# Kernel optimization log

Hardware: AMD Instinct MI355X
Metric: run time of the kernel (lower is better)

Reference implementation:

```python
import jax, jax.numpy as jnp
import numpy as np

N = 50000
E = 800000
HEADS = 4
C = 64  # per-head channels
IN = 256
NEG_SLOPE = 0.2


def setup_inputs() -> dict:
    key = jax.random.key(0)
    k = jax.random.split(key, 6)
    x = jax.random.normal(k[0], (N, IN), dtype=jnp.float32)
    edge_index = jax.random.randint(k[1], (2, E), 0, N, dtype=jnp.int64)
    # Glorot-ish scale for weights
    W = jax.random.normal(k[2], (IN, HEADS * C), dtype=jnp.float32) * (1.0 / np.sqrt(IN))
    att_src = jax.random.normal(k[3], (HEADS, C), dtype=jnp.float32) * (1.0 / np.sqrt(C))
    att_dst = jax.random.normal(k[4], (HEADS, C), dtype=jnp.float32) * (1.0 / np.sqrt(C))
    bias = jax.random.normal(k[5], (HEADS * C,), dtype=jnp.float32) * 0.02
    return {"x": x, "edge_index": edge_index, "W": W, "att_src": att_src,
            "att_dst": att_dst, "bias": bias}


def _gat_forward(x, edge_index, W, att_src, att_dst, bias):
    n = x.shape[0]
    h = (x @ W).reshape(n, HEADS, C)  # [N, H, C]

    # add self loops (PyG default add_self_loops=True)
    loop = jnp.arange(n, dtype=edge_index.dtype)
    src = jnp.concatenate([edge_index[0], loop])  # [E+N]
    dst = jnp.concatenate([edge_index[1], loop])

    # per-node attention contributions  [N, H]
    a_src = jnp.einsum('nhc,hc->nh', h, att_src)
    a_dst = jnp.einsum('nhc,hc->nh', h, att_dst)

    # edge logits with leaky relu  [E+N, H]
    logits = a_src[src] + a_dst[dst]
    logits = jnp.where(logits >= 0, logits, NEG_SLOPE * logits)

    # segment softmax over destination neighborhoods
    seg_max = jax.ops.segment_max(logits, dst, num_segments=n)  # [N, H]
    seg_max = jnp.where(jnp.isfinite(seg_max), seg_max, 0.0)
    ex = jnp.exp(logits - seg_max[dst])
    denom = jax.ops.segment_sum(ex, dst, num_segments=n)  # [N, H]
    alpha = ex / (denom[dst] + 1e-16)  # [E+N, H]

    # weighted scatter-add of source messages
    msgs = alpha[:, :, None] * h[src]  # [E+N, H, C]
    out = jax.ops.segment_sum(msgs, dst, num_segments=n)  # [N, H, C]
    out = out.reshape(n, HEADS * C) + bias
    return jax.nn.relu(out)


def reference(x, edge_index, W, att_src, att_dst, bias):
    return _gat_forward(x, edge_index, W, att_src, att_dst, bias)
```

## Files before the change

### kernel.cpp

```cpp
#include <hip/hip_runtime.h>
#include <hip/hip_bf16.h>
#include <math.h>

#define NEG 0.2f
#define BSH 6
#define EPB 2048

typedef __attribute__((ext_vector_type(4))) float f4;
typedef __attribute__((ext_vector_type(8))) short s8;

__device__ __forceinline__ short f2bf(float f) {
    unsigned u = __float_as_uint(f);
    u += 0x7fff + ((u >> 16) & 1);
    return (short)(u >> 16);
}
__device__ __forceinline__ unsigned pk2(float a, float b) {
    union { __hip_bfloat162 h; unsigned u; } c;
    c.h = __float22bfloat162_rn(make_float2(a, b));
    return c.u;
}
__device__ __forceinline__ float bf2f(unsigned short s) {
    return __uint_as_float(((unsigned)s) << 16);
}

__global__ __launch_bounds__(256) void prep_count(
    const float* __restrict__ W, short* __restrict__ Wt, int* __restrict__ off,
    const int* __restrict__ ei, int* __restrict__ hist2d,
    int E, int N, int NBUCK, int NB, int Etot)
{
    const int blk = blockIdx.x, t = threadIdx.x;
    if (blk < 256) {
        int id = blk * 256 + t;
        int n = id >> 8, k = id & 255;
        Wt[id] = f2bf(W[k * 256 + n]);
        if (id == 0) off[N] = Etot;
        return;
    }
    extern __shared__ int lh[];
    const int cblk = blk - 256;
    for (int b = t; b < NBUCK; b += 256) lh[b] = 0;
    __syncthreads();
    const int e0 = cblk * EPB;
    if (e0 + EPB <= E) {
#pragma unroll
        for (int i = 0; i < EPB / 1024; ++i) {
            int e = e0 + i * 1024 + t * 4;
            int4 d = *(const int4*)(ei + E + e);
            atomicAdd(&lh[d.x >> BSH], 1);
            atomicAdd(&lh[d.y >> BSH], 1);
            atomicAdd(&lh[d.z >> BSH], 1);
            atomicAdd(&lh[d.w >> BSH], 1);
        }
    } else {
        for (int i = 0; i < EPB / 256; ++i) {
            int e = e0 + i * 256 + t;
            if (e < Etot) {
                int dte = (e < E) ? ei[E + e] : (e - E);
                atomicAdd(&lh[dte >> BSH], 1);
            }
        }
    }
    __syncthreads();
    for (int b = t; b < NBUCK; b += 256) hist2d[b * NB + cblk] = lh[b];
}

__global__ __launch_bounds__(1024) void scan1(const int* __restrict__ src,
                                              int* __restrict__ dstT,
                                              int* __restrict__ bsum,
                                              int Ntot, int NB, int NBUCK)
{
    __shared__ int wsum[16], wexc[16];
    const int t = threadIdx.x, lane = t & 63, w = t >> 6;
    const int idx = blockIdx.x * 1024 + t;
    int v = (idx < Ntot) ? src[idx] : 0;
    int val = v;
#pragma unroll
    for (int o = 1; o < 64; o <<= 1) {
        int u = __shfl_up(val, o);
        if (lane >= o) val += u;
    }
    if (lane == 63) wsum[w] = val;
    __syncthreads();
    if (t < 16) {
        int s = wsum[t];
#pragma unroll
        for (int o = 1; o < 16; o <<= 1) {
            int u = __shfl_up(s, o, 16);
            if (t >= o) s += u;
        }
        wexc[t] = s - wsum[t];
        if (t == 15) bsum[blockIdx.x] = s;
    }
    __syncthreads();
    if (idx < Ntot) {
        int b = idx / NB, cblk = idx - b * NB;
        dstT[(size_t)cblk * NBUCK + b] = wexc[w] + val - v;
    }
}

__device__ __forceinline__ void bexc_scan_wave(const int* __restrict__ bsum,
                                               int* bexc_l, int NCH, int t)
{
    if (t < 64) {
        int carry = 0;
        for (int base = 0; base < NCH; base += 64) {
            int i = base + t;
            int v = (i < NCH) ? bsum[i] : 0;
            int val = v;
#pragma unroll
            for (int o = 1; o < 64; o <<= 1) {
                int u = __shfl_up(val, o);
                if (t >= o) val += u;
            }
            if (i < NCH) bexc_l[i] = carry + val - v;
            carry += __shfl(val, 63);
        }
    }
}

__global__ __launch_bounds__(512) void gemm_scatter(
    const float* __restrict__ x, const short* __restrict__ Wt,
    const float* __restrict__ att_src, const float* __restrict__ att_dst,
    short* __restrict__ hb, float* __restrict__ a_src_n,
    float* __restrict__ a_dst_n, int M, int GB,
    const int* __restrict__ ei, const int* __restrict__ scannedT,
    const int* __restrict__ bsum, unsigned* __restrict__ bucketed,
    int E, int N, int NBUCK, int NB, int NCH)
{
    extern __shared__ __align__(16) char smem[];
    const int t = threadIdx.x;

    if (blockIdx.x >= GB) {
        int* bexc_l = (int*)smem;
        int* lcur   = (int*)smem + 384;
        const int cblk = blockIdx.x - GB;
        bexc_scan_wave(bsum, bexc_l, NCH, t);
        __syncthreads();
        const int* srow = scannedT + (size_t)cblk * NBUCK;
        for (int b = t; b < NBUCK; b += 512)
            lcur[b] = srow[b] + bexc_l[(b * NB + cblk) >> 10];
        __syncthreads();
        const int e0 = cblk * EPB, Etot = E + N;
        if (e0 + EPB <= E) {
            int e = e0 + t * 4;
            int4 s4 = *(const int4*)(ei + e);
            int4 d4 = *(const int4*)(ei + E + e);
            int p0 = atomicAdd(&lcur[d4.x >> BSH], 1);
            bucketed[p0] = (unsigned)s4.x | ((unsigned)(d4.x & 63) << 20);
            int p1 = atomicAdd(&lcur[d4.y >> BSH], 1);
            bucketed[p1] = (unsigned)s4.y | ((unsigned)(d4.y & 63) << 20);
            int p2 = atomicAdd(&lcur[d4.z >> BSH], 1);
            bucketed[p2] = (unsigned)s4.z | ((unsigned)(d4.z & 63) << 20);
            int p3 = atomicAdd(&lcur[d4.w >> BSH], 1);
            bucketed[p3] = (unsigned)s4.w | ((unsigned)(d4.w & 63) << 20);
        } else {
            for (int i = 0; i < EPB / 512; ++i) {
                int e = e0 + i * 512 + t;
                if (e < Etot) {
                    int src, dte;
                    if (e < E) { src = ei[e]; dte = ei[E + e]; }
                    else       { src = e - E; dte = src; }
                    int pos = atomicAdd(&lcur[dte >> BSH], 1);
                    bucketed[pos] = (unsigned)src | ((unsigned)(dte & 63) << 20);
                }
            }
        }
        return;
    }

    short (*xs)[128][32] = (short (*)[128][32])smem;
    const int lane = t & 63, wv = t >> 6;
    const int wr = wv >> 2;
    const int hd = wv & 3;
    const int quad = lane >> 4, l15 = lane & 15;
    const int n0 = blockIdx.x * 128;

    const int row = t >> 2, kq = t & 3;
    const bool okr = (n0 + row) < M;
    const float* xp = x + (size_t)(n0 + row) * 256 + kq * 8;

    const short* wbase = Wt + (size_t)(hd * 64 + l15) * 256 + quad * 8;

    f4 acc[4][4];
#pragma unroll
    for (int i = 0; i < 4; ++i)
#pragma unroll
        for (int j = 0; j < 4; ++j) acc[i][j] = (f4)(0.f);

    float4 v0 = {}, v1 = {};
    if (okr) { const float4* p = (const float4*)xp; v0 = p[0]; v1 = p[1]; }

    s8 af[4];
#pragma unroll
    for (int i = 0; i < 4; ++i)
        af[i] = *(const s8*)(wbase + (size_t)(i * 16) * 256);

    int buf = 0;
#pragma unroll
    for (int ks = 0; ks < 8; ++ks) {
        uint4 u = { pk2(v0.x, v0.y), pk2(v0.z, v0.w), pk2(v1.x, v1.y), pk2(v1.z, v1.w) };
        *(uint4*)&xs[buf][row][kq * 8] = u;
        __syncthreads();

        if (ks < 7 && okr) {
            const float4* p = (const float4*)(xp + (ks + 1) * 32);
            v0 = p[0]; v1 = p[1];
        }

        s8 afn[4];
        if (ks < 7) {
#pragma unroll
            for (int i = 0; i < 4; ++i)
                afn[i] = *(const s8*)(wbase + (size_t)(i * 16) * 256 + (ks + 1) * 32);
        }

        s8 bf[4];
#pragma unroll
        for (int j = 0; j < 4; ++j)
            bf[j] = *(const s8*)&xs[buf][wr * 64 + j * 16 + l15][quad * 8];
#pragma unroll
        for (int i = 0; i < 4; ++i)
#pragma unroll
            for (int j = 0; j < 4; ++j)
                acc[i][j] = __builtin_amdgcn_mfma_f32_16x16x32_bf16(af[i], bf[j], acc[i][j], 0, 0, 0);

        if (ks < 7) {
#pragma unroll
            for (int i = 0; i < 4; ++i) af[i] = afn[i];
        }
        buf ^= 1;
    }

    float asv[4][4], adv[4][4];
#pragma unroll
    for (int i = 0; i < 4; ++i)
#pragma unroll
        for (int rr = 0; rr < 4; ++rr) {
            asv[i][rr] = att_src[hd * 64 + i * 16 + quad * 4 + rr];
            adv[i][rr] = att_dst[hd * 64 + i * 16 + quad * 4 + rr];
        }

#pragma unroll
    for (int j = 0; j < 4; ++j) {
        const int node = n0 + wr * 64 + j * 16 + l15;
        const bool ok = node < M;
        float ps = 0.f, pd = 0.f;
#pragma unroll
        for (int i = 0; i < 4; ++i)
#pragma unroll
            for (int rr = 0; rr < 4; ++rr) {
                float v = acc[i][j][rr];
                ps = fmaf(v, asv[i][rr], ps);
                pd = fmaf(v, adv[i][rr], pd);
            }
        ps += __shfl_xor(ps, 16); ps += __shfl_xor(ps, 32);
        pd += __shfl_xor(pd, 16); pd += __shfl_xor(pd, 32);
        if (ok && quad == 0) {
            a_src_n[node * 4 + hd] = ps;
            a_dst_n[node * 4 + hd] = pd;
        }
        if (ok) {
#pragma unroll
            for (int i = 0; i < 4; ++i) {
                uint2 pk = make_uint2(pk2(acc[i][j][0], acc[i][j][1]),
                                      pk2(acc[i][j][2], acc[i][j][3]));
                *(uint2*)&hb[(size_t)node * 256 + hd * 64 + i * 16 + quad * 4] = pk;
            }
        }
    }
}

__global__ __launch_bounds__(512) void csr_build(
    const unsigned* __restrict__ bucketed, const int* __restrict__ scannedT,
    const int* __restrict__ bsum, int* __restrict__ off, int* __restrict__ csr,
    int N, int NB, int NBUCK, int Etot, int NCH)
{
    __shared__ unsigned est[2048];
    __shared__ int ldeg8[8][64], lcur8[8][64], loff[64], bexc_l[384];
    const int t = threadIdx.x, wv = t >> 6, b = blockIdx.x;

    bexc_scan_wave(bsum, bexc_l, NCH, t);
    ldeg8[t >> 6][t & 63] = 0;
    __syncthreads();

    const int gbase = scannedT[b] + bexc_l[(b * NB) >> 10];
    int gend;
    if (b + 1 == NBUCK) gend = Etot;
    else gend = scannedT[b + 1] + bexc_l[((b + 1) * NB) >> 10];
    int cnt = gend - gbase;
    if (cnt > 2048) cnt = 2048;

    for (int i = t; i < cnt; i += 512) {
        unsigned en = bucketed[gbase + i];
        est[i] = en;
        atomicAdd(&ldeg8[wv][en >> 20], 1);
    }
    __syncthreads();
    if (t < 64) {
        int d0 = ldeg8[0][t], d1 = ldeg8[1][t], d2 = ldeg8[2][t], d3 = ldeg8[3][t];
        int d4 = ldeg8[4][t], d5 = ldeg8[5][t], d6 = ldeg8[6][t], d7 = ldeg8[7][t];
        int tot = d0 + d1 + d2 + d3 + d4 + d5 + d6 + d7;
        int val = tot;
#pragma unroll
        for (int o = 1; o < 64; o <<= 1) {
            int u = __shfl_up(val, o);
            if (t >= o) val += u;
        }
        int excl = val - tot;
        loff[t] = excl;
        int c = excl;
        lcur8[0][t] = c; c += d0;
        lcur8[1][t] = c; c += d1;
        lcur8[2][t] = c; c += d2;
        lcur8[3][t] = c; c += d3;
        lcur8[4][t] = c; c += d4;
        lcur8[5][t] = c; c += d5;
        lcur8[6][t] = c; c += d6;
        lcur8[7][t] = c;
    }
    __syncthreads();
    for (int i = t; i < cnt; i += 512) {
        unsigned en = est[i];
        int pos = atomicAdd(&lcur8[wv][en >> 20], 1);
        csr[gbase + pos] = (int)(en & 0xFFFFF);
    }
    if (t < 64) {
        int n = (b << BSH) + t;
        if (n < N) off[n] = gbase + loff[t];
    }
}

__global__ __launch_bounds__(256) void aggregate(const short* __restrict__ hb,
                                                 const float* __restrict__ a_src_n,
                                                 const float* __restrict__ a_dst_n,
                                                 const int* __restrict__ off,
                                                 const int* __restrict__ csr,
                                                 const float* __restrict__ bias,
                                                 float* __restrict__ out, int N)
{
    __shared__ float lds_w[4][64][4];
    __shared__ int   lds_s[4][64];
    const int wv = threadIdx.x >> 6;
    const int lane = threadIdx.x & 63;
    const int half = lane >> 5, l31 = lane & 31;
    const int n = blockIdx.x * 4 + wv;
    if (n >= N) return;

    const int base = off[n];
    const int d = off[n + 1] - base;
    const float4 ad = *(const float4*)(a_dst_n + 4 * n);
    const int hl = l31 >> 3;

    float acc[8] = {0.f, 0.f, 0.f, 0.f, 0.f, 0.f, 0.f, 0.f};
    float4 sum = make_float4(0.f, 0.f, 0.f, 0.f);
    const uint4* hp = (const uint4*)hb;

    for (int c0 = 0; c0 < d; c0 += 64) {
        int j = c0 + lane;
        int s = 0;
        float4 w4 = make_float4(0.f, 0.f, 0.f, 0.f);
        if (j < d) {
            s = csr[base + j];
            float4 as = *(const float4*)(a_src_n + 4 * s);
            float lx = as.x + ad.x; lx = lx >= 0.f ? lx : NEG * lx;
            float ly = as.y + ad.y; ly = ly >= 0.f ? ly : NEG * ly;
            float lz = as.z + ad.z; lz = lz >= 0.f ? lz : NEG * lz;
            float lw = as.w + ad.w; lw = lw >= 0.f ? lw : NEG * lw;
            w4 = make_float4(__expf(lx), __expf(ly), __expf(lz), __expf(lw));
        }
        sum.x += w4.x; sum.y += w4.y; sum.z += w4.z; sum.w += w4.w;
        *(float4*)&lds_w[wv][lane][0] = w4;
        lds_s[wv][lane] = s;
        __builtin_amdgcn_wave_barrier();

        const int cl = (d - c0) < 64 ? (d - c0) : 64;
        int jj = 0;
        for (; jj + 4 <= cl; jj += 4) {
            int   s0 = lds_s[wv][jj + half];
            int   s1 = lds_s[wv][jj + 2 + half];
            float w0 = lds_w[wv][jj + half][hl];
            float w1 = lds_w[wv][jj + 2 + half][hl];
            uint4 v0 = hp[(size_t)s0 * 32 + l31];
            uint4 v1 = hp[(size_t)s1 * 32 + l31];
            acc[0] = fmaf(w0, bf2f((unsigned short)(v0.x & 0xffff)), acc[0]);
            acc[1] = fmaf(w0, bf2f((unsigned short)(v0.x >> 16)),    acc[1]);
            acc[2] = fmaf(w0, bf2f((unsigned short)(v0.y & 0xffff)), acc[2]);
            acc[3] = fmaf(w0, bf2f((unsigned short)(v0.y >> 16)),    acc[3]);
            acc[4] = fmaf(w0, bf2f((unsigned short)(v0.z & 0xffff)), acc[4]);
            acc[5] = fmaf(w0, bf2f((unsigned short)(v0.z >> 16)),    acc[5]);
            acc[6] = fmaf(w0, bf2f((unsigned short)(v0.w & 0xffff)), acc[6]);
            acc[7] = fmaf(w0, bf2f((unsigned short)(v0.w >> 16)),    acc[7]);
            acc[0] = fmaf(w1, bf2f((unsigned short)(v1.x & 0xffff)), acc[0]);
            acc[1] = fmaf(w1, bf2f((unsigned short)(v1.x >> 16)),    acc[1]);
            acc[2] = fmaf(w1, bf2f((unsigned short)(v1.y & 0xffff)), acc[2]);
            acc[3] = fmaf(w1, bf2f((unsigned short)(v1.y >> 16)),    acc[3]);
            acc[4] = fmaf(w1, bf2f((unsigned short)(v1.z & 0xffff)), acc[4]);
            acc[5] = fmaf(w1, bf2f((unsigned short)(v1.z >> 16)),    acc[5]);
            acc[6] = fmaf(w1, bf2f((unsigned short)(v1.w & 0xffff)), acc[6]);
            acc[7] = fmaf(w1, bf2f((unsigned short)(v1.w >> 16)),    acc[7]);
        }
        for (; jj < cl; jj += 2) {
            int   s0 = lds_s[wv][jj + half];
            float w0 = lds_w[wv][jj + half][hl];
            uint4 v0 = hp[(size_t)s0 * 32 + l31];
            acc[0] = fmaf(w0, bf2f((unsigned short)(v0.x & 0xffff)), acc[0]);
            acc[1] = fmaf(w0, bf2f((unsigned short)(v0.x >> 16)),    acc[1]);
            acc[2] = fmaf(w0, bf2f((unsigned short)(v0.y & 0xffff)), acc[2]);
            acc[3] = fmaf(w0, bf2f((unsigned short)(v0.y >> 16)),    acc[3]);
            acc[4] = fmaf(w0, bf2f((unsigned short)(v0.z & 0xffff)), acc[4]);
            acc[5] = fmaf(w0, bf2f((unsigned short)(v0.z >> 16)),    acc[5]);
            acc[6] = fmaf(w0, bf2f((unsigned short)(v0.w & 0xffff)), acc[6]);
            acc[7] = fmaf(w0, bf2f((unsigned short)(v0.w >> 16)),    acc[7]);
        }
        __builtin_amdgcn_wave_barrier();
    }

#pragma unroll
    for (int k = 0; k < 8; ++k) acc[k] += __shfl_xor(acc[k], 32);

#pragma unroll
    for (int o = 32; o > 0; o >>= 1) {
        sum.x += __shfl_xor(sum.x, o);
        sum.y += __shfl_xor(sum.y, o);
        sum.z += __shfl_xor(sum.z, o);
        sum.w += __shfl_xor(sum.w, o);
    }
    float sh = (hl & 2) ? ((hl & 1) ? sum.w : sum.z) : ((hl & 1) ? sum.y : sum.x);
    float ih = 1.f / (sh + 1e-16f);

    if (half == 0) {
        const float4* bp = (const float4*)bias + l31 * 2;
        float4 b0 = bp[0], b1 = bp[1];
        float4 o0, o1;
        o0.x = fmaxf(fmaf(acc[0], ih, b0.x), 0.f);
        o0.y = fmaxf(fmaf(acc[1], ih, b0.y), 0.f);
        o0.z = fmaxf(fmaf(acc[2], ih, b0.z), 0.f);
        o0.w = fmaxf(fmaf(acc[3], ih, b0.w), 0.f);
        o1.x = fmaxf(fmaf(acc[4], ih, b1.x), 0.f);
        o1.y = fmaxf(fmaf(acc[5], ih, b1.y), 0.f);
        o1.z = fmaxf(fmaf(acc[6], ih, b1.z), 0.f);
        o1.w = fmaxf(fmaf(acc[7], ih, b1.w), 0.f);
        float4* op = (float4*)(out + (size_t)n * 256) + l31 * 2;
        op[0] = o0;
        op[1] = o1;
    }
}

extern "C" void kernel_launch(void* const* d_in, const int* in_sizes, int n_in,
                              void* d_out, int out_size, void* d_ws, size_t ws_size,
                              hipStream_t stream)
{
    const float* x       = (const float*)d_in[0];
    const int*   ei      = (const int*)d_in[1];
    const float* W       = (const float*)d_in[2];
    const float* att_src = (const float*)d_in[3];
    const float* att_dst = (const float*)d_in[4];
    const float* bias    = (const float*)d_in[5];
    float* out = (float*)d_out;

    const int N = in_sizes[0] / 256;
    const int E = in_sizes[1] / 2;
    const int Etot = E + N;
    const int NBUCK = (N + 63) >> BSH;
    const int NB = (Etot + EPB - 1) / EPB;
    const int Ntot = NBUCK * NB;
    const int NCH = (Ntot + 1023) / 1024;
    const int GB = (N + 127) / 128;

    char* p = (char*)d_ws;
    short*    hb      = (short*)p;    p += (size_t)N * 256 * sizeof(short);
    short*    Wt      = (short*)p;    p += 256 * 256 * sizeof(short);
    float*    a_src_n = (float*)p;    p += (size_t)N * 4 * sizeof(float);
    float*    a_dst_n = (float*)p;    p += (size_t)N * 4 * sizeof(float);
    int*      hist2d  = (int*)p;      p += (size_t)Ntot * sizeof(int);
    int*      scannedT= (int*)p;      p += (size_t)Ntot * sizeof(int);
    int*      bsum    = (int*)p;      p += 1024 * sizeof(int);
    int*      off     = (int*)p;      p += (size_t)(N + 1) * sizeof(int);
    unsigned* bucketed= (unsigned*)p; p += (size_t)Etot * sizeof(unsigned);
    int*      csr     = (int*)p;      p += (size_t)Etot * sizeof(int);

    prep_count<<<256 + NB, 256, NBUCK * sizeof(int), stream>>>(
        W, Wt, off, ei, hist2d, E, N, NBUCK, NB, Etot);
    scan1<<<NCH, 1024, 0, stream>>>(hist2d, scannedT, bsum, Ntot, NB, NBUCK);
    gemm_scatter<<<GB + NB, 512, 16384, stream>>>(
        x, Wt, att_src, att_dst, hb, a_src_n, a_dst_n, N, GB,
        ei, scannedT, bsum, bucketed, E, N, NBUCK, NB, NCH);
    csr_build<<<NBUCK, 512, 0, stream>>>(bucketed, scannedT, bsum, off, csr,
                                         N, NB, NBUCK, Etot, NCH);
    aggregate<<<(N + 3) / 4, 256, 0, stream>>>(hb, a_src_n, a_dst_n, off, csr,
                                               bias, out, N);
}
```

Baseline: 217.4 us.

## Fuse preprocessing and GEMM kernels into one cooperative persistent kernel

Replaces the four launches before aggregation (weight transpose and histogram, scan, GEMM plus scatter, CSR build) with a single cooperative kernel. The phases are separated by grid-wide syncs, and each phase's work units are distributed over a persistent grid sized from occupancy, capped at NBUCK. The scan now handles two elements per thread with 512 threads. The goal is to remove kernel launch gaps and tail effects between the small phases. The cost is grid-sync overhead, and the GEMM now runs in a persistent loop over a grid capped at NBUCK blocks rather than its own full-size launch, which may reduce parallelism. The old multi-kernel path is kept as a fallback if the cooperative launch fails.

```diff
diff --git a/kernel.cpp b/kernel.cpp
--- a/kernel.cpp
+++ b/kernel.cpp
@@ -1,6 +1,9 @@
 #include <hip/hip_runtime.h>
 #include <hip/hip_bf16.h>
+#include <hip/hip_cooperative_groups.h>
 #include <math.h>
+
+namespace cg = cooperative_groups;
 
 #define NEG 0.2f
 #define BSH 6
@@ -21,81 +24,6 @@
 }
 __device__ __forceinline__ float bf2f(unsigned short s) {
     return __uint_as_float(((unsigned)s) << 16);
-}
-
-__global__ __launch_bounds__(256) void prep_count(
-    const float* __restrict__ W, short* __restrict__ Wt, int* __restrict__ off,
-    const int* __restrict__ ei, int* __restrict__ hist2d,
-    int E, int N, int NBUCK, int NB, int Etot)
-{
-    const int blk = blockIdx.x, t = threadIdx.x;
-    if (blk < 256) {
-        int id = blk * 256 + t;
-        int n = id >> 8, k = id & 255;
-        Wt[id] = f2bf(W[k * 256 + n]);
-        if (id == 0) off[N] = Etot;
-        return;
-    }
-    extern __shared__ int lh[];
-    const int cblk = blk - 256;
-    for (int b = t; b < NBUCK; b += 256) lh[b] = 0;
-    __syncthreads();
-    const int e0 = cblk * EPB;
-    if (e0 + EPB <= E) {
-#pragma unroll
-        for (int i = 0; i < EPB / 1024; ++i) {
-            int e = e0 + i * 1024 + t * 4;
-            int4 d = *(const int4*)(ei + E + e);
-            atomicAdd(&lh[d.x >> BSH], 1);
-            atomicAdd(&lh[d.y >> BSH], 1);
-            atomicAdd(&lh[d.z >> BSH], 1);
-            atomicAdd(&lh[d.w >> BSH], 1);
-        }
-    } else {
-        for (int i = 0; i < EPB / 256; ++i) {
-            int e = e0 + i * 256 + t;
-            if (e < Etot) {
-                int dte = (e < E) ? ei[E + e] : (e - E);
-                atomicAdd(&lh[dte >> BSH], 1);
-            }
-        }
-    }
-    __syncthreads();
-    for (int b = t; b < NBUCK; b += 256) hist2d[b * NB + cblk] = lh[b];
-}
-
-__global__ __launch_bounds__(1024) void scan1(const int* __restrict__ src,
-                                              int* __restrict__ dstT,
-                                              int* __restrict__ bsum,
-                                              int Ntot, int NB, int NBUCK)
-{
-    __shared__ int wsum[16], wexc[16];
-    const int t = threadIdx.x, lane = t & 63, w = t >> 6;
-    const int idx = blockIdx.x * 1024 + t;
-    int v = (idx < Ntot) ? src[idx] : 0;
-    int val = v;
-#pragma unroll
-    for (int o = 1; o < 64; o <<= 1) {
-        int u = __shfl_up(val, o);
-        if (lane >= o) val += u;
-    }
-    if (lane == 63) wsum[w] = val;
-    __syncthreads();
-    if (t < 16) {
-        int s = wsum[t];
-#pragma unroll
-        for (int o = 1; o < 16; o <<= 1) {
-            int u = __shfl_up(s, o, 16);
-            if (t >= o) s += u;
-        }
-        wexc[t] = s - wsum[t];
-        if (t == 15) bsum[blockIdx.x] = s;
-    }
-    __syncthreads();
-    if (idx < Ntot) {
-        int b = idx / NB, cblk = idx - b * NB;
-        dstT[(size_t)cblk * NBUCK + b] = wexc[w] + val - v;
-    }
 }
 
 __device__ __forceinline__ void bexc_scan_wave(const int* __restrict__ bsum,
@@ -118,67 +46,22 @@
     }
 }
 
-__global__ __launch_bounds__(512) void gemm_scatter(
+__device__ __forceinline__ void gemm_body(
+    char* smem, int t, int n0,
     const float* __restrict__ x, const short* __restrict__ Wt,
     const float* __restrict__ att_src, const float* __restrict__ att_dst,
     short* __restrict__ hb, float* __restrict__ a_src_n,
-    float* __restrict__ a_dst_n, int M, int GB,
-    const int* __restrict__ ei, const int* __restrict__ scannedT,
-    const int* __restrict__ bsum, unsigned* __restrict__ bucketed,
-    int E, int N, int NBUCK, int NB, int NCH)
-{
-    extern __shared__ __align__(16) char smem[];
-    const int t = threadIdx.x;
-
-    if (blockIdx.x >= GB) {
-        int* bexc_l = (int*)smem;
-        int* lcur   = (int*)smem + 384;
-        const int cblk = blockIdx.x - GB;
-        bexc_scan_wave(bsum, bexc_l, NCH, t);
-        __syncthreads();
-        const int* srow = scannedT + (size_t)cblk * NBUCK;
-        for (int b = t; b < NBUCK; b += 512)
-            lcur[b] = srow[b] + bexc_l[(b * NB + cblk) >> 10];
-        __syncthreads();
-        const int e0 = cblk * EPB, Etot = E + N;
-        if (e0 + EPB <= E) {
-            int e = e0 + t * 4;
-            int4 s4 = *(const int4*)(ei + e);
-            int4 d4 = *(const int4*)(ei + E + e);
-            int p0 = atomicAdd(&lcur[d4.x >> BSH], 1);
-            bucketed[p0] = (unsigned)s4.x | ((unsigned)(d4.x & 63) << 20);
-            int p1 = atomicAdd(&lcur[d4.y >> BSH], 1);
-            bucketed[p1] = (unsigned)s4.y | ((unsigned)(d4.y & 63) << 20);
-            int p2 = atomicAdd(&lcur[d4.z >> BSH], 1);
-            bucketed[p2] = (unsigned)s4.z | ((unsigned)(d4.z & 63) << 20);
-            int p3 = atomicAdd(&lcur[d4.w >> BSH], 1);
-            bucketed[p3] = (unsigned)s4.w | ((unsigned)(d4.w & 63) << 20);
-        } else {
-            for (int i = 0; i < EPB / 512; ++i) {
-                int e = e0 + i * 512 + t;
-                if (e < Etot) {
-                    int src, dte;
-                    if (e < E) { src = ei[e]; dte = ei[E + e]; }
-                    else       { src = e - E; dte = src; }
-                    int pos = atomicAdd(&lcur[dte >> BSH], 1);
-                    bucketed[pos] = (unsigned)src | ((unsigned)(dte & 63) << 20);
-                }
-            }
-        }
-        return;
-    }
-
+    float* __restrict__ a_dst_n, int M)
+{
     short (*xs)[128][32] = (short (*)[128][32])smem;
     const int lane = t & 63, wv = t >> 6;
     const int wr = wv >> 2;
     const int hd = wv & 3;
     const int quad = lane >> 4, l15 = lane & 15;
-    const int n0 = blockIdx.x * 128;
 
     const int row = t >> 2, kq = t & 3;
     const bool okr = (n0 + row) < M;
     const float* xp = x + (size_t)(n0 + row) * 256 + kq * 8;
-
     const short* wbase = Wt + (size_t)(hd * 64 + l15) * 256 + quad * 8;
 
     f4 acc[4][4];
@@ -206,14 +89,12 @@
             const float4* p = (const float4*)(xp + (ks + 1) * 32);
             v0 = p[0]; v1 = p[1];
         }
-
         s8 afn[4];
         if (ks < 7) {
 #pragma unroll
             for (int i = 0; i < 4; ++i)
                 afn[i] = *(const s8*)(wbase + (size_t)(i * 16) * 256 + (ks + 1) * 32);
         }
-
         s8 bf[4];
 #pragma unroll
         for (int j = 0; j < 4; ++j)
@@ -223,7 +104,6 @@
 #pragma unroll
             for (int j = 0; j < 4; ++j)
                 acc[i][j] = __builtin_amdgcn_mfma_f32_16x16x32_bf16(af[i], bf[j], acc[i][j], 0, 0, 0);
-
         if (ks < 7) {
 #pragma unroll
             for (int i = 0; i < 4; ++i) af[i] = afn[i];
@@ -239,7 +119,6 @@
             asv[i][rr] = att_src[hd * 64 + i * 16 + quad * 4 + rr];
             adv[i][rr] = att_dst[hd * 64 + i * 16 + quad * 4 + rr];
         }
-
 #pragma unroll
     for (int j = 0; j < 4; ++j) {
         const int node = n0 + wr * 64 + j * 16 + l15;
@@ -270,17 +149,62 @@
     }
 }
 
-__global__ __launch_bounds__(512) void csr_build(
+__device__ __forceinline__ void scatter_body(
+    char* smem, int t, int cblk,
+    const int* __restrict__ ei, const int* __restrict__ scannedT,
+    const int* __restrict__ bsum, unsigned* __restrict__ bucketed,
+    int E, int N, int NBUCK, int NB, int NCH)
+{
+    int* bexc_l = (int*)smem;
+    int* lcur   = (int*)smem + 384;
+    bexc_scan_wave(bsum, bexc_l, NCH, t);
+    __syncthreads();
+    const int* srow = scannedT + (size_t)cblk * NBUCK;
+    for (int b = t; b < NBUCK; b += 512)
+        lcur[b] = srow[b] + bexc_l[(b * NB + cblk) >> 10];
+    __syncthreads();
+    const int e0 = cblk * EPB, Etot = E + N;
+    if (e0 + EPB <= E) {
+        int e = e0 + t * 4;
+        int4 s4 = *(const int4*)(ei + e);
+        int4 d4 = *(const int4*)(ei + E + e);
+        int p0 = atomicAdd(&lcur[d4.x >> BSH], 1);
+        bucketed[p0] = (unsigned)s4.x | ((unsigned)(d4.x & 63) << 20);
+        int p1 = atomicAdd(&lcur[d4.y >> BSH], 1);
+        bucketed[p1] = (unsigned)s4.y | ((unsigned)(d4.y & 63) << 20);
+        int p2 = atomicAdd(&lcur[d4.z >> BSH], 1);
+        bucketed[p2] = (unsigned)s4.z | ((unsigned)(d4.z & 63) << 20);
+        int p3 = atomicAdd(&lcur[d4.w >> BSH], 1);
+        bucketed[p3] = (unsigned)s4.w | ((unsigned)(d4.w & 63) << 20);
+    } else {
+        for (int i = 0; i < EPB / 512; ++i) {
+            int e = e0 + i * 512 + t;
+            if (e < Etot) {
+                int src, dte;
+                if (e < E) { src = ei[e]; dte = ei[E + e]; }
+                else       { src = e - E; dte = src; }
+                int pos = atomicAdd(&lcur[dte >> BSH], 1);
+                bucketed[pos] = (unsigned)src | ((unsigned)(dte & 63) << 20);
+            }
+        }
+    }
+}
+
+__device__ __forceinline__ void csr_body(
+    char* smem, int t, int b,
     const unsigned* __restrict__ bucketed, const int* __restrict__ scannedT,
     const int* __restrict__ bsum, int* __restrict__ off, int* __restrict__ csr,
     int N, int NB, int NBUCK, int Etot, int NCH)
 {
-    __shared__ unsigned est[2048];
-    __shared__ int ldeg8[8][64], lcur8[8][64], loff[64], bexc_l[384];
-    const int t = threadIdx.x, wv = t >> 6, b = blockIdx.x;
+    unsigned* est = (unsigned*)smem;
+    int* ldeg8  = (int*)(smem + 8192);
+    int* lcur8  = (int*)(smem + 10240);
+    int* loff   = (int*)(smem + 12288);
+    int* bexc_l = (int*)(smem + 12544);
+    const int wv = t >> 6;
 
     bexc_scan_wave(bsum, bexc_l, NCH, t);
-    ldeg8[t >> 6][t & 63] = 0;
+    ldeg8[(t >> 6) * 64 + (t & 63)] = 0;
     __syncthreads();
 
     const int gbase = scannedT[b] + bexc_l[(b * NB) >> 10];
@@ -293,12 +217,12 @@
     for (int i = t; i < cnt; i += 512) {
         unsigned en = bucketed[gbase + i];
         est[i] = en;
-        atomicAdd(&ldeg8[wv][en >> 20], 1);
+        atomicAdd(&ldeg8[wv * 64 + (en >> 20)], 1);
     }
     __syncthreads();
     if (t < 64) {
-        int d0 = ldeg8[0][t], d1 = ldeg8[1][t], d2 = ldeg8[2][t], d3 = ldeg8[3][t];
-        int d4 = ldeg8[4][t], d5 = ldeg8[5][t], d6 = ldeg8[6][t], d7 = ldeg8[7][t];
+        int d0 = ldeg8[0 * 64 + t], d1 = ldeg8[1 * 64 + t], d2 = ldeg8[2 * 64 + t], d3 = ldeg8[3 * 64 + t];
+        int d4 = ldeg8[4 * 64 + t], d5 = ldeg8[5 * 64 + t], d6 = ldeg8[6 * 64 + t], d7 = ldeg8[7 * 64 + t];
         int tot = d0 + d1 + d2 + d3 + d4 + d5 + d6 + d7;
         int val = tot;
 #pragma unroll
@@ -309,25 +233,229 @@
         int excl = val - tot;
         loff[t] = excl;
         int c = excl;
-        lcur8[0][t] = c; c += d0;
-        lcur8[1][t] = c; c += d1;
-        lcur8[2][t] = c; c += d2;
-        lcur8[3][t] = c; c += d3;
-        lcur8[4][t] = c; c += d4;
-        lcur8[5][t] = c; c += d5;
-        lcur8[6][t] = c; c += d6;
-        lcur8[7][t] = c;
+        lcur8[0 * 64 + t] = c; c += d0;
+        lcur8[1 * 64 + t] = c; c += d1;
+        lcur8[2 * 64 + t] = c; c += d2;
+        lcur8[3 * 64 + t] = c; c += d3;
+        lcur8[4 * 64 + t] = c; c += d4;
+        lcur8[5 * 64 + t] = c; c += d5;
+        lcur8[6 * 64 + t] = c; c += d6;
+        lcur8[7 * 64 + t] = c;
     }
     __syncthreads();
     for (int i = t; i < cnt; i += 512) {
         unsigned en = est[i];
-        int pos = atomicAdd(&lcur8[wv][en >> 20], 1);
+        int pos = atomicAdd(&lcur8[wv * 64 + (en >> 20)], 1);
         csr[gbase + pos] = (int)(en & 0xFFFFF);
     }
     if (t < 64) {
         int n = (b << BSH) + t;
         if (n < N) off[n] = gbase + loff[t];
     }
+}
+
+__global__ __launch_bounds__(512) void mega(
+    const float* __restrict__ x, const float* __restrict__ W,
+    short* __restrict__ Wt,
+    const float* __restrict__ att_src, const float* __restrict__ att_dst,
+    short* __restrict__ hb, float* __restrict__ a_src_n, float* __restrict__ a_dst_n,
+    const int* __restrict__ ei, int* __restrict__ hist2d, int* __restrict__ scannedT,
+    int* __restrict__ bsum, int* __restrict__ off, unsigned* __restrict__ bucketed,
+    int* __restrict__ csr,
+    int N, int E, int Etot, int NBUCK, int NB, int Ntot, int NCH, int GB)
+{
+    extern __shared__ __align__(16) char smem[];
+    cg::grid_group gg = cg::this_grid();
+    const int t = threadIdx.x;
+    const int NBLK = gridDim.x;
+
+    for (int u = blockIdx.x; u < 128 + NB; u += NBLK) {
+        __syncthreads();
+        if (u < 128) {
+            int id = u * 512 + t;
+            int n = id >> 8, k = id & 255;
+            Wt[id] = f2bf(W[k * 256 + n]);
+            if (id == 0) off[N] = Etot;
+        } else {
+            int* lh = (int*)smem;
+            const int cblk = u - 128;
+            for (int b = t; b < NBUCK; b += 512) lh[b] = 0;
+            __syncthreads();
+            const int e0 = cblk * EPB;
+            if (e0 + EPB <= E) {
+                int e = e0 + t * 4;
+                int4 d = *(const int4*)(ei + E + e);
+                atomicAdd(&lh[d.x >> BSH], 1);
+                atomicAdd(&lh[d.y >> BSH], 1);
+                atomicAdd(&lh[d.z >> BSH], 1);
+                atomicAdd(&lh[d.w >> BSH], 1);
+            } else {
+                for (int i = 0; i < EPB / 512; ++i) {
+                    int e = e0 + i * 512 + t;
+                    if (e < Etot) {
+                        int dte = (e < E) ? ei[E + e] : (e - E);
+                        atomicAdd(&lh[dte >> BSH], 1);
+                    }
+                }
+            }
+            __syncthreads();
+            for (int b = t; b < NBUCK; b += 512) hist2d[b * NB + cblk] = lh[b];
+        }
+    }
+    __threadfence();
+    gg.sync();
+
+    for (int u = blockIdx.x; u < NCH + GB; u += NBLK) {
+        __syncthreads();
+        if (u < NCH) {
+            int* wsum = (int*)smem;
+            int* wexc = (int*)smem + 8;
+            const int lane = t & 63, w = t >> 6;
+            int base = u << 10;
+            int i0 = base + 2 * t;
+            int v0 = (i0 < Ntot) ? hist2d[i0] : 0;
+            int v1 = (i0 + 1 < Ntot) ? hist2d[i0 + 1] : 0;
+            int pv = v0 + v1;
+            int val = pv;
+#pragma unroll
+            for (int o = 1; o < 64; o <<= 1) { int s2 = __shfl_up(val, o); if (lane >= o) val += s2; }
+            if (lane == 63) wsum[w] = val;
+            __syncthreads();
+            if (t < 8) {
+                int s = wsum[t];
+#pragma unroll
+                for (int o = 1; o < 8; o <<= 1) { int s2 = __shfl_up(s, o, 8); if (t >= o) s += s2; }
+                wexc[t] = s - wsum[t];
+                if (t == 7) bsum[u] = s;
+            }
+            __syncthreads();
+            int excl = wexc[w] + val - pv;
+            if (i0 < Ntot) { int b = i0 / NB, cb = i0 - b * NB; scannedT[(size_t)cb * NBUCK + b] = excl; }
+            if (i0 + 1 < Ntot) { int idx = i0 + 1; int b = idx / NB, cb = idx - b * NB; scannedT[(size_t)cb * NBUCK + b] = excl + v0; }
+        } else {
+            gemm_body(smem, t, (u - NCH) * 128, x, Wt, att_src, att_dst,
+                      hb, a_src_n, a_dst_n, N);
+        }
+    }
+    __threadfence();
+    gg.sync();
+
+    for (int u = blockIdx.x; u < NB; u += NBLK) {
+        __syncthreads();
+        scatter_body(smem, t, u, ei, scannedT, bsum, bucketed, E, N, NBUCK, NB, NCH);
+    }
+    __threadfence();
+    gg.sync();
+
+    for (int u = blockIdx.x; u < NBUCK; u += NBLK) {
+        __syncthreads();
+        csr_body(smem, t, u, bucketed, scannedT, bsum, off, csr, N, NB, NBUCK, Etot, NCH);
+    }
+}
+
+__global__ __launch_bounds__(256) void prep_count(
+    const float* __restrict__ W, short* __restrict__ Wt, int* __restrict__ off,
+    const int* __restrict__ ei, int* __restrict__ hist2d,
+    int E, int N, int NBUCK, int NB, int Etot)
+{
+    const int blk = blockIdx.x, t = threadIdx.x;
+    if (blk < 256) {
+        int id = blk * 256 + t;
+        int n = id >> 8, k = id & 255;
+        Wt[id] = f2bf(W[k * 256 + n]);
+        if (id == 0) off[N] = Etot;
+        return;
+    }
+    extern __shared__ int lh[];
+    const int cblk = blk - 256;
+    for (int b = t; b < NBUCK; b += 256) lh[b] = 0;
+    __syncthreads();
+    const int e0 = cblk * EPB;
+    if (e0 + EPB <= E) {
+#pragma unroll
+        for (int i = 0; i < EPB / 1024; ++i) {
+            int e = e0 + i * 1024 + t * 4;
+            int4 d = *(const int4*)(ei + E + e);
+            atomicAdd(&lh[d.x >> BSH], 1);
+            atomicAdd(&lh[d.y >> BSH], 1);
+            atomicAdd(&lh[d.z >> BSH], 1);
+            atomicAdd(&lh[d.w >> BSH], 1);
+        }
+    } else {
+        for (int i = 0; i < EPB / 256; ++i) {
+            int e = e0 + i * 256 + t;
+            if (e < Etot) {
+                int dte = (e < E) ? ei[E + e] : (e - E);
+                atomicAdd(&lh[dte >> BSH], 1);
+            }
+        }
+    }
+    __syncthreads();
+    for (int b = t; b < NBUCK; b += 256) hist2d[b * NB + cblk] = lh[b];
+}
+
+__global__ __launch_bounds__(1024) void scan1(const int* __restrict__ src,
+                                              int* __restrict__ dstT,
+                                              int* __restrict__ bsum,
+                                              int Ntot, int NB, int NBUCK)
+{
+    __shared__ int wsum[16], wexc[16];
+    const int t = threadIdx.x, lane = t & 63, w = t >> 6;
+    const int idx = blockIdx.x * 1024 + t;
+    int v = (idx < Ntot) ? src[idx] : 0;
+    int val = v;
+#pragma unroll
+    for (int o = 1; o < 64; o <<= 1) {
+        int u = __shfl_up(val, o);
+        if (lane >= o) val += u;
+    }
+    if (lane == 63) wsum[w] = val;
+    __syncthreads();
+    if (t < 16) {
+        int s = wsum[t];
+#pragma unroll
+        for (int o = 1; o < 16; o <<= 1) {
+            int u = __shfl_up(s, o, 16);
+            if (t >= o) s += u;
+        }
+        wexc[t] = s - wsum[t];
+        if (t == 15) bsum[blockIdx.x] = s;
+    }
+    __syncthreads();
+    if (idx < Ntot) {
+        int b = idx / NB, cblk = idx - b * NB;
+        dstT[(size_t)cblk * NBUCK + b] = wexc[w] + val - v;
+    }
+}
+
+__global__ __launch_bounds__(512) void gemm_scatter(
+    const float* __restrict__ x, const short* __restrict__ Wt,
+    const float* __restrict__ att_src, const float* __restrict__ att_dst,
+    short* __restrict__ hb, float* __restrict__ a_src_n,
+    float* __restrict__ a_dst_n, int M, int GB,
+    const int* __restrict__ ei, const int* __restrict__ scannedT,
+    const int* __restrict__ bsum, unsigned* __restrict__ bucketed,
+    int E, int N, int NBUCK, int NB, int NCH)
+{
+    extern __shared__ __align__(16) char smem2[];
+    const int t = threadIdx.x;
+    if (blockIdx.x >= GB) {
+        scatter_body(smem2, t, blockIdx.x - GB, ei, scannedT, bsum, bucketed,
+                     E, N, NBUCK, NB, NCH);
+        return;
+    }
+    gemm_body(smem2, t, blockIdx.x * 128, x, Wt, att_src, att_dst,
+              hb, a_src_n, a_dst_n, M);
+}
+
+__global__ __launch_bounds__(512) void csr_build(
+    const unsigned* __restrict__ bucketed, const int* __restrict__ scannedT,
+    const int* __restrict__ bsum, int* __restrict__ off, int* __restrict__ csr,
+    int N, int NB, int NBUCK, int Etot, int NCH)
+{
+    extern __shared__ __align__(16) char smem3[];
+    csr_body(smem3, threadIdx.x, blockIdx.x, bucketed, scannedT, bsum, off, csr,
+             N, NB, NBUCK, Etot, NCH);
 }
 
 __global__ __launch_bounds__(256) void aggregate(const short* __restrict__ hb,
@@ -479,14 +607,41 @@
     unsigned* bucketed= (unsigned*)p; p += (size_t)Etot * sizeof(unsigned);
     int*      csr     = (int*)p;      p += (size_t)Etot * sizeof(int);
 
-    prep_count<<<256 + NB, 256, NBUCK * sizeof(int), stream>>>(
-        W, Wt, off, ei, hist2d, E, N, NBUCK, NB, Etot);
-    scan1<<<NCH, 1024, 0, stream>>>(hist2d, scannedT, bsum, Ntot, NB, NBUCK);
-    gemm_scatter<<<GB + NB, 512, 16384, stream>>>(
-        x, Wt, att_src, att_dst, hb, a_src_n, a_dst_n, N, GB,
-        ei, scannedT, bsum, bucketed, E, N, NBUCK, NB, NCH);
-    csr_build<<<NBUCK, 512, 0, stream>>>(bucketed, scannedT, bsum, off, csr,
-                                         N, NB, NBUCK, Etot, NCH);
+    static int s_coopGrid = -1;
+    if (s_coopGrid < 0) {
+        int nb = 0;
+        hipError_t qe = hipOccupancyMaxActiveBlocksPerMultiprocessor(&nb, mega, 512,
+                                                                     (size_t)16384);
+        if (qe != hipSuccess || nb < 1) nb = 1;
+        int g = nb * 256;
+        if (g > NBUCK) g = NBUCK;
+        s_coopGrid = g;
+    }
+
+    const float* x_ = x; const float* W_ = W; short* Wt_ = Wt;
+    const float* as_ = att_src; const float* ad_ = att_dst;
+    short* hb_ = hb; float* asn_ = a_src_n; float* adn_ = a_dst_n;
+    const int* ei_ = ei; int* h2_ = hist2d; int* sT_ = scannedT;
+    int* bs_ = bsum; int* off_ = off; unsigned* bk_ = bucketed; int* csr_ = csr;
+    int N_ = N, E_ = E, Etot_ = Etot, NBUCK_ = NBUCK, NB_ = NB,
+        Ntot_ = Ntot, NCH_ = NCH, GB_ = GB;
+    void* margs[] = { &x_, &W_, &Wt_, &as_, &ad_, &hb_, &asn_, &adn_, &ei_,
+                      &h2_, &sT_, &bs_, &off_, &bk_, &csr_,
+                      &N_, &E_, &Etot_, &NBUCK_, &NB_, &Ntot_, &NCH_, &GB_ };
+
+    hipError_t ce = hipLaunchCooperativeKernel(mega, dim3(s_coopGrid), dim3(512),
+                                               margs, 16384, stream);
+    if (ce != hipSuccess) {
+        (void)hipGetLastError();
+        prep_count<<<256 + NB, 256, NBUCK * sizeof(int), stream>>>(
+            W, Wt, off, ei, hist2d, E, N, NBUCK, NB, Etot);
+        scan1<<<NCH, 1024, 0, stream>>>(hist2d, scannedT, bsum, Ntot, NB, NBUCK);
+        gemm_scatter<<<GB + NB, 512, 16384, stream>>>(
+            x, Wt, att_src, att_dst, hb, a_src_n, a_dst_n, N, GB,
+            ei, scannedT, bsum, bucketed, E, N, NBUCK, NB, NCH);
+        csr_build<<<NBUCK, 512, 16384, stream>>>(bucketed, scannedT, bsum, off, csr,
+                                                 N, NB, NBUCK, Etot, NCH);
+    }
     aggregate<<<(N + 3) / 4, 256, 0, stream>>>(hb, a_src_n, a_dst_n, off, csr,
                                                bias, out, N);
 }
```

Result: slower. 536.6 us (+146.9%).
